# Optimization experiments

Measured on AMD Instinct MI355X. Metric: run time of the kernel, lower is better.

Reference implementation:

```python
import jax, jax.numpy as jnp
import numpy as np

FACTOR = 5  # init factor


def setup_inputs() -> dict:
    key = jax.random.key(0)
    k1, k2, k3, k4 = jax.random.split(key, 4)
    B, H, L, D = 4, 8, 2048, 64
    sample_k = min(FACTOR * int(np.ceil(np.log(L))), L)  # 40
    queries = jax.random.normal(k1, (B, H, L, D), dtype=jnp.float32)
    keys = jax.random.normal(k2, (B, H, L, D), dtype=jnp.float32)
    values = jax.random.normal(k3, (B, H, L, D), dtype=jnp.float32)
    index_sample = jax.random.randint(k4, (L, sample_k), 0, L)
    return {"queries": queries, "keys": keys, "values": values,
            "index_sample": index_sample}


def reference(queries, keys, values, index_sample):
    B, H, L_Q, D = queries.shape
    L_K = keys.shape[2]
    n_top = min(FACTOR * int(np.ceil(np.log(L_Q))), L_Q)

    # --- _prob_QK ---
    # Gather sampled keys per query position: [B,H,L_Q,sample_k,D]
    K_sample = keys[:, :, index_sample, :]
    # Q.unsqueeze(3) @ K_sample^T -> [B,H,L_Q,sample_k]
    Q_K_sample = jnp.einsum('bhld,bhlsd->bhls', queries, K_sample)
    # sparsity measure M = max - mean
    M = Q_K_sample.max(axis=-1) - Q_K_sample.sum(axis=-1) / L_K
    _, M_top = jax.lax.top_k(M, n_top)  # [B,H,n_top]
    # gather top queries: [B,H,n_top,D]
    Q_reduce = jnp.take_along_axis(queries, M_top[..., None], axis=2)
    # full scores for top queries: [B,H,n_top,L_K]
    scores_top = jnp.einsum('bhud,bhkd->bhuk', Q_reduce, keys)

    # --- scale ---
    scale = 1.0 / np.sqrt(D).astype(np.float32)
    scores_top = scores_top * scale

    # --- initial context (mask_flag=False): mean of V broadcast over L_Q ---
    V_mean = values.mean(axis=2)  # [B,H,D]
    context = jnp.broadcast_to(V_mean[:, :, None, :], (B, H, L_Q, D))

    # --- update context at top-query positions ---
    attn = jax.nn.softmax(scores_top, axis=-1)           # [B,H,n_top,L_K]
    ctx_update = jnp.einsum('bhuk,bhkd->bhud', attn, values)
    b_idx = jnp.arange(B)[:, None, None]
    h_idx = jnp.arange(H)[None, :, None]
    context = context.at[b_idx, h_idx, M_top].set(ctx_update)
    return context
```

## Files before the change

### kernel.cpp

```cpp
#include <hip/hip_runtime.h>
#include <math.h>

#define BH 32
#define L  2048
#define D  64
#define SK 40
#define NT 40
#define NC 32
#define CK 64
#define SP 65
#define SCALE 0.125f

#define WS_M      0
#define WS_MTOP   262144
#define WS_VP     267264
#define WS_VM     529408
#define WS_QTOP   537600
#define WS_OPART  865280
#define WS_MPART  11351040
#define WS_LPART  11514880

template <int CTRL>
__device__ __forceinline__ float dpp_add(float x) {
    int y = __builtin_amdgcn_update_dpp(0, __float_as_int(x), CTRL, 0xF, 0xF, true);
    return x + __int_as_float(y);
}

__global__ __launch_bounds__(512) void kMV(const float* __restrict__ Q,
                                           const float* __restrict__ K,
                                           const float* __restrict__ V,
                                           const int* __restrict__ idx,
                                           float* __restrict__ M,
                                           float* __restrict__ Vp)
{
    __shared__ int   sidx[64 * SK];
    __shared__ float red[512];

    int t    = threadIdx.x;
    int b    = blockIdx.x;
    int head = ((b >> 3) & 3) * 8 + (b & 7);
    int qc   = b >> 5;
    int l0   = qc * 64;

    {
        int d = t & 63, r = t >> 6;
        const float* Vb = V + ((size_t)head * L + l0 + r * 8) * D + d;
        float acc = 0.f;
        #pragma unroll
        for (int k = 0; k < 8; ++k) acc += Vb[(size_t)k * D];
        red[t] = acc;
    }
    for (int i = t; i < 64 * SK; i += 512) sidx[i] = idx[l0 * SK + i];
    __syncthreads();
    if (t < 64) {
        float s = 0.f;
        #pragma unroll
        for (int rr = 0; rr < 8; ++rr) s += red[t + rr * 64];
        Vp[(head * 32 + qc) * 64 + t] = s;
    }

    int wave = t >> 6, lane = t & 63;
    int g  = lane >> 3;
    int dl = lane & 7;
    int lq = wave * 8 + g;
    size_t qid = (size_t)head * L + (l0 + lq);

    const float4* Q4 = reinterpret_cast<const float4*>(Q);
    float4 q0 = Q4[qid * 16 + dl * 2 + 0];
    float4 q1 = Q4[qid * 16 + dl * 2 + 1];
    const float4* Kb4 = reinterpret_cast<const float4*>(K) + (size_t)head * L * 16;

    float mx = -INFINITY, sm = 0.f;
    #pragma unroll 4
    for (int s = 0; s < SK; ++s) {
        int kr = sidx[lq * SK + s];
        const float4* kp = Kb4 + (size_t)kr * 16 + dl * 2;
        float4 k0 = kp[0], k1 = kp[1];
        float p = q0.x * k0.x + q0.y * k0.y + q0.z * k0.z + q0.w * k0.w
                + q1.x * k1.x + q1.y * k1.y + q1.z * k1.z + q1.w * k1.w;
        p = dpp_add<0xB1>(p);
        p = dpp_add<0x4E>(p);
        p = dpp_add<0x12C>(p);
        mx = fmaxf(mx, p);
        sm += p;
    }
    if (dl == 0) M[qid] = mx - sm * (1.0f / (float)L);
}

__global__ __launch_bounds__(256) void kTopVm(const float* __restrict__ M,
                                              const float* __restrict__ Vp,
                                              const float* __restrict__ Q,
                                              int* __restrict__ Mtop,
                                              float* __restrict__ Vm,
                                              float* __restrict__ Qtop)
{
    __shared__ unsigned int keys[L];
    __shared__ int hist[256];
    __shared__ int wtot[4];
    __shared__ unsigned int pref_s;
    __shared__ int krem_s;
    __shared__ int cnt_gt, cnt_eq;
    __shared__ int eqlist[64];
    __shared__ int stop[NT];

    int bh = blockIdx.x;
    int t  = threadIdx.x;
    int lane = t & 63, w = t >> 6;

    if (t < 64) {
        float s = 0.f;
        #pragma unroll
        for (int c = 0; c < 32; ++c) s += Vp[(bh * 32 + c) * 64 + t];
        Vm[bh * D + t] = s * (1.0f / (float)L);
    }

    for (int i = t; i < L; i += 256) {
        unsigned int u = __float_as_uint(M[bh * L + i]);
        keys[i] = (u & 0x80000000u) ? ~u : (u | 0x80000000u);
    }
    if (t == 0) { pref_s = 0u; krem_s = NT; cnt_gt = 0; cnt_eq = 0; }
    __syncthreads();

    #pragma unroll
    for (int shift = 24; shift >= 0; shift -= 8) {
        hist[t] = 0;
        __syncthreads();
        unsigned int pref = pref_s;
        int krem = krem_s;
        for (int i = t; i < L; i += 256) {
            unsigned int k  = keys[i];
            unsigned int hi = (shift == 24) ? 0u : (k >> (shift + 8));
            if (hi == pref) atomicAdd(&hist[(k >> shift) & 0xFF], 1);
        }
        __syncthreads();
        int h = hist[t];
        int v = h;
        #pragma unroll
        for (int o = 1; o < 64; o <<= 1) {
            int u = __shfl_down(v, o, 64);
            if (lane + o < 64) v += u;
        }
        if (lane == 0) wtot[w] = v;
        __syncthreads();
        int ss = v;
        #pragma unroll
        for (int w2 = 1; w2 < 4; ++w2) if (w2 > w) ss += wtot[w2];
        if (ss - h < krem && ss >= krem) {
            krem_s = krem - (ss - h);
            pref_s = (pref << 8) | (unsigned int)t;
        }
    }
    __syncthreads();

    unsigned int T = pref_s;
    int krem = krem_s;
    for (int i = t; i < L; i += 256) {
        unsigned int k = keys[i];
        if (k > T) {
            int p = atomicAdd(&cnt_gt, 1);
            Mtop[bh * NT + p] = i;
            stop[p] = i;
        } else if (k == T) {
            int p = atomicAdd(&cnt_eq, 1);
            if (p < 64) eqlist[p] = i;
        }
    }
    __syncthreads();
    if (t == 0) {
        int base = cnt_gt;
        int m = cnt_eq < 64 ? cnt_eq : 64;
        for (int q = 0; q < krem; ++q) {
            int best = 0x7fffffff, bj = -1;
            for (int j = 0; j < m; ++j) if (eqlist[j] < best) { best = eqlist[j]; bj = j; }
            Mtop[bh * NT + base + q] = best;
            stop[base + q] = best;
            if (bj >= 0) eqlist[bj] = 0x7fffffff;
        }
    }
    __syncthreads();
    const float4* Qg = reinterpret_cast<const float4*>(Q) + (size_t)bh * L * 16;
    float4* Qt = reinterpret_cast<float4*>(Qtop) + (size_t)bh * NT * 16;
    for (int i = t; i < NT * 16; i += 256)
        Qt[i] = Qg[(size_t)stop[i >> 4] * 16 + (i & 15)];
}

__global__ __launch_bounds__(256) void kAttnPart(const float* __restrict__ Qtop,
                                                 const float* __restrict__ K,
                                                 const float* __restrict__ V,
                                                 const float* __restrict__ Vm,
                                                 float* __restrict__ Opart,
                                                 float* __restrict__ mpart,
                                                 float* __restrict__ lpart,
                                                 float* __restrict__ out)
{
    __shared__ float4 V4s[CK * 16];
    __shared__ float  S[NT * SP];
    __shared__ float  smax[NT], ssum[NT];

    int c = blockIdx.x, bh = blockIdx.y;
    int t = threadIdx.x;

    {
        const float4* Vm4 = reinterpret_cast<const float4*>(Vm + bh * D);
        float4* outB = reinterpret_cast<float4*>(out) + ((size_t)bh * L + c * CK) * 16;
        #pragma unroll
        for (int k = 0; k < 4; ++k) { int i = t + k * 256; outB[i] = Vm4[i & 15]; }
    }

    const float4* Vg = reinterpret_cast<const float4*>(V) + ((size_t)bh * L + c * CK) * 16;
    float4 vreg[4];
    #pragma unroll
    for (int k = 0; k < 4; ++k) vreg[k] = Vg[t + k * 256];

    int w    = __builtin_amdgcn_readfirstlane(t) >> 6;
    int lane = t & 63;
    const float4* Kg = reinterpret_cast<const float4*>(K) + ((size_t)bh * L + c * CK) * 16;
    float4 k[16];
    #pragma unroll
    for (int d4 = 0; d4 < 16; ++d4) k[d4] = Kg[(size_t)lane * 16 + d4];

    const float4* Qb = reinterpret_cast<const float4*>(Qtop) + ((size_t)bh * NT + w * 10) * 16;
    float p[10];
    #pragma unroll
    for (int i = 0; i < 10; ++i) {
        float a0 = 0.f;
        #pragma unroll
        for (int d4 = 0; d4 < 16; ++d4) {
            float4 q4 = Qb[i * 16 + d4];
            a0 += q4.x * k[d4].x + q4.y * k[d4].y + q4.z * k[d4].z + q4.w * k[d4].w;
        }
        p[i] = a0 * SCALE;
    }

    #pragma unroll
    for (int i = 0; i < 10; ++i) {
        int u = w * 10 + i;
        float m = p[i];
        #pragma unroll
        for (int o = 1; o < 64; o <<= 1) m = fmaxf(m, __shfl_xor(m, o, 64));
        float e = __expf(p[i] - m);
        float l2 = e;
        #pragma unroll
        for (int o = 1; o < 64; o <<= 1) l2 += __shfl_xor(l2, o, 64);
        S[u * SP + lane] = e;
        if (lane == 0) { smax[u] = m; ssum[u] = l2; }
    }

    #pragma unroll
    for (int kk = 0; kk < 4; ++kk) {
        int i = t + kk * 256;
        int j = i >> 4, d4 = i & 15;
        V4s[j * 16 + (d4 ^ (j & 15))] = vreg[kk];
    }
    __syncthreads();

    {
        int a = t >> 5, r = t & 31;
        int d4 = r >> 1, jh = r & 1;
        float4 acc[5];
        #pragma unroll
        for (int ui = 0; ui < 5; ++ui) acc[ui] = make_float4(0.f, 0.f, 0.f, 0.f);
        for (int jj = 0; jj < 32; ++jj) {
            int j = jh * 32 + jj;
            float4 v4 = V4s[j * 16 + (d4 ^ (j & 15))];
            #pragma unroll
            for (int ui = 0; ui < 5; ++ui) {
                float pw = S[(a + 8 * ui) * SP + j];
                acc[ui].x += pw * v4.x; acc[ui].y += pw * v4.y;
                acc[ui].z += pw * v4.z; acc[ui].w += pw * v4.w;
            }
        }
        #pragma unroll
        for (int ui = 0; ui < 5; ++ui) {
            acc[ui].x = dpp_add<0xB1>(acc[ui].x);
            acc[ui].y = dpp_add<0xB1>(acc[ui].y);
            acc[ui].z = dpp_add<0xB1>(acc[ui].z);
            acc[ui].w = dpp_add<0xB1>(acc[ui].w);
        }
        if (jh == 0) {
            float4* Og = reinterpret_cast<float4*>(Opart) + ((size_t)(bh * NC + c) * NT) * 16;
            #pragma unroll
            for (int ui = 0; ui < 5; ++ui)
                Og[(a + 8 * ui) * 16 + d4] = acc[ui];
        }
    }
    if (t < NT) {
        mpart[(bh * NC + c) * NT + t] = smax[t];
        lpart[(bh * NC + c) * NT + t] = ssum[t];
    }
}

__global__ __launch_bounds__(64) void kCombine(const float* __restrict__ Opart,
                                               const float* __restrict__ mpart,
                                               const float* __restrict__ lpart,
                                               const int* __restrict__ Mtop,
                                               float* __restrict__ out)
{
    int u = blockIdx.x, bh = blockIdx.y, d = threadIdx.x;
    float gm = -INFINITY;
    #pragma unroll
    for (int c = 0; c < NC; ++c) gm = fmaxf(gm, mpart[(bh * NC + c) * NT + u]);
    float den = 0.f, o = 0.f;
    #pragma unroll
    for (int c = 0; c < NC; ++c) {
        int pi = (bh * NC + c) * NT + u;
        float wgt = __expf(mpart[pi] - gm);
        den += wgt * lpart[pi];
        o   += wgt * Opart[(size_t)pi * D + d];
    }
    int qrow = Mtop[bh * NT + u];
    out[((size_t)bh * L + qrow) * D + d] = o / den;
}

extern "C" void kernel_launch(void* const* d_in, const int* in_sizes, int n_in,
                              void* d_out, int out_size, void* d_ws, size_t ws_size,
                              hipStream_t stream)
{
    const float* Q   = (const float*)d_in[0];
    const float* K   = (const float*)d_in[1];
    const float* V   = (const float*)d_in[2];
    const int*   idx = (const int*)d_in[3];
    float* out = (float*)d_out;

    char* ws = (char*)d_ws;
    float* M     = (float*)(ws + WS_M);
    int*   Mtop  = (int*)  (ws + WS_MTOP);
    float* Vp    = (float*)(ws + WS_VP);
    float* Vm    = (float*)(ws + WS_VM);
    float* Qtop  = (float*)(ws + WS_QTOP);
    float* Opart = (float*)(ws + WS_OPART);
    float* mpart = (float*)(ws + WS_MPART);
    float* lpart = (float*)(ws + WS_LPART);

    kMV      <<<1024, 512, 0, stream>>>(Q, K, V, idx, M, Vp);
    kTopVm   <<<BH, 256, 0, stream>>>(M, Vp, Q, Mtop, Vm, Qtop);
    kAttnPart<<<dim3(NC, BH), 256, 0, stream>>>(Qtop, K, V, Vm, Opart, mpart, lpart, out);
    kCombine <<<dim3(NT, BH), 64, 0, stream>>>(Opart, mpart, lpart, Mtop, out);
}
```

Before: 164.4 us.

## Stream each head's K through LDS in chunks instead of random gathers

The sampled-QK kernel no longer gathers the 40 sampled key rows per query straight from global memory. Each block now streams the whole head's K matrix through shared memory in 16 coalesced chunks of 128 rows, prefetching the next chunk into registers while the current one is used. Per chunk, each query group finds its sampled indices that fall in that chunk with a ballot bitmask and computes those dot products from LDS. This trades scattered global reads for a full-K sweep per block, plus 32 extra barriers, a divergent per-chunk loop and higher LDS use that may lower occupancy.

```diff
diff --git a/kernel.cpp b/kernel.cpp
--- a/kernel.cpp
+++ b/kernel.cpp
@@ -11,6 +11,10 @@
 #define SP 65
 #define SCALE 0.125f
 
+#define KCH   16
+#define KROWS 128
+#define KST   68
+
 #define WS_M      0
 #define WS_MTOP   262144
 #define WS_VP     267264
@@ -33,6 +37,7 @@
                                            float* __restrict__ M,
                                            float* __restrict__ Vp)
 {
+    __shared__ float Ks[KROWS * KST];
     __shared__ int   sidx[64 * SK];
     __shared__ float red[512];
 
@@ -51,7 +56,14 @@
         red[t] = acc;
     }
     for (int i = t; i < 64 * SK; i += 512) sidx[i] = idx[l0 * SK + i];
-    __syncthreads();
+
+    const float4* Kg4 = reinterpret_cast<const float4*>(K) + (size_t)head * L * 16;
+    float4 vk[4];
+    #pragma unroll
+    for (int kk = 0; kk < 4; ++kk) vk[kk] = Kg4[t + kk * 512];
+
+    __syncthreads();
+
     if (t < 64) {
         float s = 0.f;
         #pragma unroll
@@ -68,21 +80,49 @@
     const float4* Q4 = reinterpret_cast<const float4*>(Q);
     float4 q0 = Q4[qid * 16 + dl * 2 + 0];
     float4 q1 = Q4[qid * 16 + dl * 2 + 1];
-    const float4* Kb4 = reinterpret_cast<const float4*>(K) + (size_t)head * L * 16;
+
+    int sid[5];
+    #pragma unroll
+    for (int j = 0; j < 5; ++j) sid[j] = sidx[lq * SK + 8 * j + dl];
 
     float mx = -INFINITY, sm = 0.f;
-    #pragma unroll 4
-    for (int s = 0; s < SK; ++s) {
-        int kr = sidx[lq * SK + s];
-        const float4* kp = Kb4 + (size_t)kr * 16 + dl * 2;
-        float4 k0 = kp[0], k1 = kp[1];
-        float p = q0.x * k0.x + q0.y * k0.y + q0.z * k0.z + q0.w * k0.w
-                + q1.x * k1.x + q1.y * k1.y + q1.z * k1.z + q1.w * k1.w;
-        p = dpp_add<0xB1>(p);
-        p = dpp_add<0x4E>(p);
-        p = dpp_add<0x12C>(p);
-        mx = fmaxf(mx, p);
-        sm += p;
+
+    for (int c = 0; c < KCH; ++c) {
+        __syncthreads();
+        #pragma unroll
+        for (int kk = 0; kk < 4; ++kk) {
+            int i = t + kk * 512, row = i >> 4, d4 = i & 15;
+            *reinterpret_cast<float4*>(&Ks[row * KST + d4 * 4]) = vk[kk];
+        }
+        if (c < KCH - 1) {
+            #pragma unroll
+            for (int kk = 0; kk < 4; ++kk)
+                vk[kk] = Kg4[(c + 1) * (KROWS * 16) + t + kk * 512];
+        }
+        __syncthreads();
+
+        unsigned long long m40 = 0ull;
+        #pragma unroll
+        for (int j = 0; j < 5; ++j) {
+            bool hit = (sid[j] >> 7) == c;
+            unsigned long long bal = __ballot(hit);
+            m40 |= ((bal >> (g * 8)) & 0xFFull) << (8 * j);
+        }
+        while (m40) {
+            int s = __builtin_ctzll(m40);
+            m40 &= m40 - 1;
+            int kslot = sidx[lq * SK + s] & (KROWS - 1);
+            const float* kr = &Ks[kslot * KST + dl * 8];
+            float4 k0 = *reinterpret_cast<const float4*>(kr);
+            float4 k1 = *reinterpret_cast<const float4*>(kr + 4);
+            float p = q0.x * k0.x + q0.y * k0.y + q0.z * k0.z + q0.w * k0.w
+                    + q1.x * k1.x + q1.y * k1.y + q1.z * k1.z + q1.w * k1.w;
+            p = dpp_add<0xB1>(p);
+            p = dpp_add<0x4E>(p);
+            p = dpp_add<0x12C>(p);
+            mx = fmaxf(mx, p);
+            sm += p;
+        }
     }
     if (dl == 0) M[qid] = mx - sm * (1.0f / (float)L);
 }
```

New measurement: 298.4 us. 81.6% more time.
